# Optimization experiments

Measured on AMD Instinct MI355X. Metric: run time of the kernel, lower is better.

## Reference

```python
import jax, jax.numpy as jnp
import numpy as np

# SAT factor-graph sizes: V variables, F clauses (functions), E edges (3-SAT: E = 3*F)
V = 2000
F = 8400
E = 25200
EPS = 1e-40
MAX_LOGIT = 30.0
PI = 0.0  # pi init kwarg

def safe_log(x):
    return jnp.log(jnp.maximum(x, EPS))

def safe_exp(x):
    return jnp.exp(jnp.minimum(x, MAX_LOGIT))

def setup_inputs() -> dict:
    key = jax.random.key(0)
    ks = jax.random.split(key, 8)
    # each edge connects exactly one variable and one clause
    var_idx = jax.random.randint(ks[0], (E,), 0, V)
    func_idx = jax.random.randint(ks[1], (E,), 0, F)
    edge_feature = (2 * jax.random.randint(ks[2], (E, 1), 0, 2) - 1).astype(jnp.float32)  # +/-1 literal polarity
    variable_mask_T = jax.nn.one_hot(var_idx, V, dtype=jnp.float32)          # [E,V]
    function_mask = jax.nn.one_hot(func_idx, F, dtype=jnp.float32).T        # [F,E]
    p_variable_mask = (variable_mask_T * (edge_feature > 0)).T               # [V,E], positive literals
    n_variable_mask = (variable_mask_T * (edge_feature < 0)).T               # [V,E], negative literals
    # init_state per get_init_state(randomized=True)
    vs = jax.random.uniform(ks[3], (E, 3), dtype=jnp.float32)
    variable_state = vs / vs.sum(1, keepdims=True)
    function_state = jnp.concatenate([jax.random.uniform(ks[4], (E, 1), dtype=jnp.float32), jnp.zeros((E, 1), jnp.float32)], 1)
    dvs = jax.random.uniform(ks[5], (E, 3), dtype=jnp.float32)
    decimator_variable_state = dvs / dvs.sum(1, keepdims=True)
    decimator_function_state = jnp.concatenate([jax.random.uniform(ks[6], (E, 1), dtype=jnp.float32, minval=0.05, maxval=0.95), jnp.zeros((E, 1), jnp.float32)], 1)
    return {
        'variable_state': variable_state,
        'function_state': function_state,
        'decimator_variable_state': decimator_variable_state,
        'decimator_function_state': decimator_function_state,
        'variable_mask_T': variable_mask_T,
        'function_mask': function_mask,
        'p_variable_mask': p_variable_mask,
        'n_variable_mask': n_variable_mask,
        'edge_feature': edge_feature,
    }

def reference(variable_state, function_state, decimator_variable_state, decimator_function_state,
              variable_mask_T, function_mask, p_variable_mask, n_variable_mask, edge_feature):
    # active_mask is None -> mask = ones(E,1); edge_mask is None (decimator_state has length 2)
    mask = jnp.ones((edge_feature.shape[0], 1), dtype=jnp.float32)
    # --- function update: clause-side aggregation of log messages ---
    dvs = safe_log(decimator_variable_state[:, :1])                 # [E,1]
    agg = function_mask.T @ (function_mask @ dvs) - dvs             # sum over clause, minus self
    function_state_new = mask * safe_exp(agg) + (1 - mask) * function_state[:, :1]
    # --- variable update ---
    external_force = decimator_function_state[:, 1:2]               # [E,1]
    dfs = safe_log(1.0 - decimator_function_state[:, :1])           # [E,1]
    pos = variable_mask_T @ (p_variable_mask @ dfs)                 # [E,1]
    neg = variable_mask_T @ (n_variable_mask @ dfs)                 # [E,1]
    ef = edge_feature
    same_sign = 0.5 * (1 + ef) * pos + 0.5 * (1 - ef) * neg - dfs
    same_sign = same_sign + safe_log(1.0 - PI * (external_force == ef).astype(jnp.float32))
    opposite_sign = 0.5 * (1 - ef) * pos + 0.5 * (1 + ef) * neg
    opposite_sign = opposite_sign + safe_log(1.0 - PI * (external_force == -ef).astype(jnp.float32))
    dont_care = safe_exp(same_sign + opposite_sign)
    same_sign = safe_exp(same_sign)
    opposite_sign = safe_exp(opposite_sign)
    q_u = same_sign * (1 - opposite_sign)
    q_s = opposite_sign * (1 - same_sign)
    total = q_u + q_s + dont_care
    temp = jnp.concatenate([q_u, q_s, dont_care], 1) / total        # [E,3]
    variable_state_new = mask * temp + (1 - mask) * variable_state
    return (variable_state_new, jnp.concatenate([function_state_new, external_force], 1))
```

## Files before the change

kernel.cpp:

```cpp
#include <hip/hip_runtime.h>

#define NV 2000
#define NF 8400
#define NE 25200

__device__ __forceinline__ float safe_log(float x) {
    return __logf(fmaxf(x, 1e-40f));
}
__device__ __forceinline__ float safe_exp(float x) {
    return __expf(fminf(x, 30.0f));
}

__global__ void k_prep(const float* __restrict__ dec_var,
                       const float* __restrict__ dec_func,
                       float* __restrict__ dvs, float* __restrict__ dfs,
                       float* __restrict__ fsum,
                       float* __restrict__ psum, float* __restrict__ nsum)
{
    unsigned i = blockIdx.x * blockDim.x + threadIdx.x;
    unsigned stride = gridDim.x * blockDim.x;
    for (unsigned e = i; e < NE; e += stride) {
        dvs[e] = safe_log(dec_var[e * 3]);
        dfs[e] = safe_log(1.0f - dec_func[e * 2]);
    }
    for (unsigned f = i; f < NF; f += stride) fsum[f] = 0.0f;
    for (unsigned v = i; v < NV; v += stride) { psum[v] = 0.0f; nsum[v] = 0.0f; }
}

__global__ void k_scan_var(const float4* __restrict__ vmT,
                           const float* __restrict__ dfs,
                           const float* __restrict__ ef,
                           int* __restrict__ var_idx,
                           float* __restrict__ psum, float* __restrict__ nsum)
{
    const unsigned total = NE * NV / 4u;
    unsigned i = blockIdx.x * blockDim.x + threadIdx.x;
    unsigned stride = gridDim.x * blockDim.x;
    for (; i < total; i += stride) {
        float4 x = vmT[i];
        if (x.x != 0.f || x.y != 0.f || x.z != 0.f || x.w != 0.f) {
            unsigned lin = i * 4u;
            unsigned e = lin / NV;
            unsigned v = lin - e * NV;
            v += (x.x != 0.f) ? 0u : (x.y != 0.f) ? 1u : (x.z != 0.f) ? 2u : 3u;
            var_idx[e] = (int)v;
            float d = dfs[e];
            if (ef[e] > 0.f) atomicAdd(&psum[v], d);
            else             atomicAdd(&nsum[v], d);
        }
    }
}

__global__ void k_scan_func(const float4* __restrict__ fm,
                            const float* __restrict__ dvs,
                            int* __restrict__ func_idx,
                            float* __restrict__ fsum)
{
    const unsigned total = NF * NE / 4u;
    unsigned i = blockIdx.x * blockDim.x + threadIdx.x;
    unsigned stride = gridDim.x * blockDim.x;
    for (; i < total; i += stride) {
        float4 x = fm[i];
        if (x.x != 0.f || x.y != 0.f || x.z != 0.f || x.w != 0.f) {
            unsigned lin = i * 4u;
            unsigned f = lin / NE;
            unsigned e0 = lin - f * NE;
            float acc = 0.f;
            if (x.x != 0.f) { func_idx[e0 + 0] = (int)f; acc += dvs[e0 + 0]; }
            if (x.y != 0.f) { func_idx[e0 + 1] = (int)f; acc += dvs[e0 + 1]; }
            if (x.z != 0.f) { func_idx[e0 + 2] = (int)f; acc += dvs[e0 + 2]; }
            if (x.w != 0.f) { func_idx[e0 + 3] = (int)f; acc += dvs[e0 + 3]; }
            atomicAdd(&fsum[f], acc);
        }
    }
}

__global__ void k_final(const float* __restrict__ dvs, const float* __restrict__ dfs,
                        const int* __restrict__ var_idx, const int* __restrict__ func_idx,
                        const float* __restrict__ fsum,
                        const float* __restrict__ psum, const float* __restrict__ nsum,
                        const float* __restrict__ ef,
                        const float* __restrict__ dec_func,
                        float* __restrict__ out)
{
    unsigned i = blockIdx.x * blockDim.x + threadIdx.x;
    unsigned stride = gridDim.x * blockDim.x;
    for (unsigned e = i; e < NE; e += stride) {
        float d_vs = dvs[e];
        float d_fs = dfs[e];
        float agg = fsum[func_idx[e]] - d_vs;
        float fstate = safe_exp(agg);
        float extf = dec_func[e * 2 + 1];

        int v = var_idx[e];
        float p = psum[v], n = nsum[v];
        float f = ef[e];
        float ss_log = ((f > 0.f) ? p : n) - d_fs;
        float os_log = ((f > 0.f) ? n : p);
        float dc = safe_exp(ss_log + os_log);
        float ss = safe_exp(ss_log);
        float os = safe_exp(os_log);
        float qu = ss * (1.f - os);
        float qs = os * (1.f - ss);
        float inv = 1.f / (qu + qs + dc);

        out[e * 3 + 0] = qu * inv;
        out[e * 3 + 1] = qs * inv;
        out[e * 3 + 2] = dc * inv;
        out[NE * 3 + e * 2 + 0] = fstate;
        out[NE * 3 + e * 2 + 1] = extf;
    }
}

extern "C" void kernel_launch(void* const* d_in, const int* in_sizes, int n_in,
                              void* d_out, int out_size, void* d_ws, size_t ws_size,
                              hipStream_t stream) {
    const float* dec_var  = (const float*)d_in[2];
    const float* dec_func = (const float*)d_in[3];
    const float* vmT      = (const float*)d_in[4];
    const float* fm       = (const float*)d_in[5];
    const float* ef       = (const float*)d_in[8];
    float* out = (float*)d_out;

    float* ws = (float*)d_ws;
    float* dvs      = ws;
    float* dfs      = ws + NE;
    int*   var_idx  = (int*)(ws + 2 * NE);
    int*   func_idx = (int*)(ws + 3 * NE);
    float* fsum     = ws + 4 * NE;
    float* psum     = fsum + NF;
    float* nsum     = psum + NV;

    k_prep<<<128, 256, 0, stream>>>(dec_var, dec_func, dvs, dfs, fsum, psum, nsum);
    k_scan_var<<<2048, 256, 0, stream>>>((const float4*)vmT, dfs, ef, var_idx, psum, nsum);
    k_scan_func<<<2048, 256, 0, stream>>>((const float4*)fm, dvs, func_idx, fsum);
    k_final<<<128, 256, 0, stream>>>(dvs, dfs, var_idx, func_idx, fsum, psum, nsum,
                                     ef, dec_func, out);
}
```

Baseline: 192.9 us.

## Merge both mask scans into one kernel with nontemporal unrolled loads

```diff
diff --git a/kernel.cpp b/kernel.cpp
--- a/kernel.cpp
+++ b/kernel.cpp
@@ -4,11 +4,16 @@
 #define NF 8400
 #define NE 25200
 
+typedef float f32x4 __attribute__((ext_vector_type(4)));
+
 __device__ __forceinline__ float safe_log(float x) {
     return __logf(fmaxf(x, 1e-40f));
 }
 __device__ __forceinline__ float safe_exp(float x) {
     return __expf(fminf(x, 30.0f));
+}
+__device__ __forceinline__ f32x4 ntload(const f32x4* __restrict__ p) {
+    return __builtin_nontemporal_load(p);
 }
 
 __global__ void k_prep(const float* __restrict__ dec_var,
@@ -27,51 +32,87 @@
     for (unsigned v = i; v < NV; v += stride) { psum[v] = 0.0f; nsum[v] = 0.0f; }
 }
 
-__global__ void k_scan_var(const float4* __restrict__ vmT,
-                           const float* __restrict__ dfs,
-                           const float* __restrict__ ef,
-                           int* __restrict__ var_idx,
-                           float* __restrict__ psum, float* __restrict__ nsum)
+
+__device__ __forceinline__ void proc_fm(f32x4 x, unsigned i,
+                                        const float* __restrict__ dvs,
+                                        int* __restrict__ func_idx,
+                                        float* __restrict__ fsum)
 {
-    const unsigned total = NE * NV / 4u;
-    unsigned i = blockIdx.x * blockDim.x + threadIdx.x;
-    unsigned stride = gridDim.x * blockDim.x;
-    for (; i < total; i += stride) {
-        float4 x = vmT[i];
-        if (x.x != 0.f || x.y != 0.f || x.z != 0.f || x.w != 0.f) {
-            unsigned lin = i * 4u;
-            unsigned e = lin / NV;
-            unsigned v = lin - e * NV;
-            v += (x.x != 0.f) ? 0u : (x.y != 0.f) ? 1u : (x.z != 0.f) ? 2u : 3u;
-            var_idx[e] = (int)v;
-            float d = dfs[e];
-            if (ef[e] > 0.f) atomicAdd(&psum[v], d);
-            else             atomicAdd(&nsum[v], d);
-        }
+    if (x.x != 0.f || x.y != 0.f || x.z != 0.f || x.w != 0.f) {
+        unsigned lin = i * 4u;
+        unsigned f = lin / NE;
+        unsigned e0 = lin - f * NE;
+        float acc = 0.f;
+        if (x.x != 0.f) { func_idx[e0 + 0] = (int)f; acc += dvs[e0 + 0]; }
+        if (x.y != 0.f) { func_idx[e0 + 1] = (int)f; acc += dvs[e0 + 1]; }
+        if (x.z != 0.f) { func_idx[e0 + 2] = (int)f; acc += dvs[e0 + 2]; }
+        if (x.w != 0.f) { func_idx[e0 + 3] = (int)f; acc += dvs[e0 + 3]; }
+        atomicAdd(&fsum[f], acc);
     }
 }
 
-__global__ void k_scan_func(const float4* __restrict__ fm,
-                            const float* __restrict__ dvs,
-                            int* __restrict__ func_idx,
-                            float* __restrict__ fsum)
+__device__ __forceinline__ void proc_vm(f32x4 x, unsigned i,
+                                        const float* __restrict__ dfs,
+                                        const float* __restrict__ ef,
+                                        int* __restrict__ var_idx,
+                                        float* __restrict__ psum,
+                                        float* __restrict__ nsum)
 {
-    const unsigned total = NF * NE / 4u;
-    unsigned i = blockIdx.x * blockDim.x + threadIdx.x;
-    unsigned stride = gridDim.x * blockDim.x;
-    for (; i < total; i += stride) {
-        float4 x = fm[i];
-        if (x.x != 0.f || x.y != 0.f || x.z != 0.f || x.w != 0.f) {
-            unsigned lin = i * 4u;
-            unsigned f = lin / NE;
-            unsigned e0 = lin - f * NE;
-            float acc = 0.f;
-            if (x.x != 0.f) { func_idx[e0 + 0] = (int)f; acc += dvs[e0 + 0]; }
-            if (x.y != 0.f) { func_idx[e0 + 1] = (int)f; acc += dvs[e0 + 1]; }
-            if (x.z != 0.f) { func_idx[e0 + 2] = (int)f; acc += dvs[e0 + 2]; }
-            if (x.w != 0.f) { func_idx[e0 + 3] = (int)f; acc += dvs[e0 + 3]; }
-            atomicAdd(&fsum[f], acc);
+    if (x.x != 0.f || x.y != 0.f || x.z != 0.f || x.w != 0.f) {
+        unsigned lin = i * 4u;
+        unsigned e = lin / NV;
+        unsigned v = lin - e * NV;
+        v += (x.x != 0.f) ? 0u : (x.y != 0.f) ? 1u : (x.z != 0.f) ? 2u : 3u;
+        var_idx[e] = (int)v;
+        float d = dfs[e];
+        if (ef[e] > 0.f) atomicAdd(&psum[v], d);
+        else             atomicAdd(&nsum[v], d);
+    }
+}
+
+#define FM_BLOCKS 2100u
+#define VM_BLOCKS 500u
+#define SCAN_BLOCKS (FM_BLOCKS + VM_BLOCKS)
+
+__global__ void k_scan(const f32x4* __restrict__ fm, const f32x4* __restrict__ vmT,
+                       const float* __restrict__ dvs, const float* __restrict__ dfs,
+                       const float* __restrict__ ef,
+                       int* __restrict__ func_idx, int* __restrict__ var_idx,
+                       float* __restrict__ fsum,
+                       float* __restrict__ psum, float* __restrict__ nsum)
+{
+    if (blockIdx.x < FM_BLOCKS) {
+        const unsigned total = NF * NE / 4u;
+        const unsigned stride = FM_BLOCKS * 256u;
+        unsigned i = blockIdx.x * 256u + threadIdx.x;
+        for (; i + 3u * stride < total; i += 4u * stride) {
+            f32x4 a = ntload(fm + i);
+            f32x4 b = ntload(fm + i + stride);
+            f32x4 c = ntload(fm + i + 2u * stride);
+            f32x4 d = ntload(fm + i + 3u * stride);
+            proc_fm(a, i,               dvs, func_idx, fsum);
+            proc_fm(b, i + stride,      dvs, func_idx, fsum);
+            proc_fm(c, i + 2u * stride, dvs, func_idx, fsum);
+            proc_fm(d, i + 3u * stride, dvs, func_idx, fsum);
         }
+        for (; i < total; i += stride)
+            proc_fm(ntload(fm + i), i, dvs, func_idx, fsum);
+    } else {
+        const unsigned total = NE * NV / 4u;
+        const unsigned stride = VM_BLOCKS * 256u;
+        unsigned i = (blockIdx.x - FM_BLOCKS) * 256u + threadIdx.x;
+        for (; i + 3u * stride < total; i += 4u * stride) {
+            f32x4 a = ntload(vmT + i);
+            f32x4 b = ntload(vmT + i + stride);
+            f32x4 c = ntload(vmT + i + 2u * stride);
+            f32x4 d = ntload(vmT + i + 3u * stride);
+            proc_vm(a, i,               dfs, ef, var_idx, psum, nsum);
+            proc_vm(b, i + stride,      dfs, ef, var_idx, psum, nsum);
+            proc_vm(c, i + 2u * stride, dfs, ef, var_idx, psum, nsum);
+            proc_vm(d, i + 3u * stride, dfs, ef, var_idx, psum, nsum);
+        }
+        for (; i < total; i += stride)
+            proc_vm(ntload(vmT + i), i, dfs, ef, var_idx, psum, nsum);
     }
 }
 
@@ -132,8 +173,9 @@
     float* nsum     = psum + NV;
 
     k_prep<<<128, 256, 0, stream>>>(dec_var, dec_func, dvs, dfs, fsum, psum, nsum);
-    k_scan_var<<<2048, 256, 0, stream>>>((const float4*)vmT, dfs, ef, var_idx, psum, nsum);
-    k_scan_func<<<2048, 256, 0, stream>>>((const float4*)fm, dvs, func_idx, fsum);
+    k_scan<<<SCAN_BLOCKS, 256, 0, stream>>>((const f32x4*)fm, (const f32x4*)vmT,
+                                            dvs, dfs, ef, func_idx, var_idx,
+                                            fsum, psum, nsum);
     k_final<<<128, 256, 0, stream>>>(dvs, dfs, var_idx, func_idx, fsum, psum, nsum,
                                      ef, dec_func, out);
 }
```

Measured after the change: 187.0 us. 3.0% less time.
